# Kernel optimization log

Measured on AMD Instinct MI355X. Metric: run time of the kernel, lower is better.

## Reference

```python
import jax, jax.numpy as jnp
import numpy as np

B, C, H, W_SP = 4, 64, 64, 64
CI = C // 2  # inter_channels = 32
DEPTH = 64
EPS = 1e-5


def conv2d(x, w, b, pad=0, dil=1):
    out = jax.lax.conv_general_dilated(
        x, w, window_strides=(1, 1),
        padding=[(pad, pad), (pad, pad)],
        rhs_dilation=(dil, dil),
        dimension_numbers=('NCHW', 'OIHW', 'NCHW'))
    return out + b[None, :, None, None]


def setup_inputs() -> dict:
    key = jax.random.key(0)
    ks = iter(jax.random.split(key, 32))
    nrm = lambda shp, s=0.01: jax.random.normal(next(ks), shp, jnp.float32) * s
    inp = {
        'x': jax.random.normal(next(ks), (B, C, H, W_SP), jnp.float32),
        # NonlocalBlock params (init: normal(0, 0.01), bias 0)
        'g_w': nrm((CI, C, 1, 1)), 'g_b': jnp.zeros((CI,), jnp.float32),
        'theta_w': nrm((CI, C, 1, 1)), 'theta_b': jnp.zeros((CI,), jnp.float32),
        'phi_w': nrm((CI, C, 1, 1)), 'phi_b': jnp.zeros((CI,), jnp.float32),
        'Wz_w': nrm((C, CI, 1, 1)), 'Wz_b': jnp.zeros((C,), jnp.float32),
        'bn_g': jax.random.normal(next(ks), (C,), jnp.float32),  # normal_(W[1].weight, 0) -> std 1
        'bn_b': jnp.zeros((C,), jnp.float32),
        # ASPP params (torch default kaiming init approximated by small normals)
        'a_mean_w': nrm((DEPTH, C, 1, 1), 0.05), 'a_mean_b': jnp.zeros((DEPTH,), jnp.float32),
        'a1_w': nrm((DEPTH, C, 1, 1), 0.05), 'a1_b': jnp.zeros((DEPTH,), jnp.float32),
        'a3_w': nrm((DEPTH, C, 3, 3), 0.02), 'a3_b': jnp.zeros((DEPTH,), jnp.float32),
        'a5_w': nrm((DEPTH, C, 3, 3), 0.02), 'a5_b': jnp.zeros((DEPTH,), jnp.float32),
        'a7_w': nrm((DEPTH, C, 3, 3), 0.02), 'a7_b': jnp.zeros((DEPTH,), jnp.float32),
        'out_w': nrm((DEPTH, DEPTH * 5, 1, 1), 0.02), 'out_b': jnp.zeros((DEPTH,), jnp.float32),
    }
    return inp


def _forward(x, g_w, g_b, theta_w, theta_b, phi_w, phi_b, Wz_w, Wz_b, bn_g, bn_b,
             a_mean_w, a_mean_b, a1_w, a1_b, a3_w, a3_b, a5_w, a5_b, a7_w, a7_b,
             out_w, out_b):
    b, c, h, w = x.shape
    n = h * w
    # ---- NonlocalBlock: global self-attention ----
    g_x = conv2d(x, g_w, g_b).reshape(b, CI, n).transpose(0, 2, 1)       # [B,N,Ci]
    theta_x = conv2d(x, theta_w, theta_b).reshape(b, CI, n).transpose(0, 2, 1)  # [B,N,Ci]
    phi_x = conv2d(x, phi_w, phi_b).reshape(b, CI, n)                    # [B,Ci,N]
    f = jnp.einsum('bqc,bck->bqk', theta_x, phi_x)                       # [B,N,N]
    f_div_C = jax.nn.softmax(f, axis=2)
    y = jnp.einsum('bqk,bkc->bqc', f_div_C, g_x)                         # [B,N,Ci]
    y = y.transpose(0, 2, 1).reshape(b, CI, h, w)
    wy = conv2d(y, Wz_w, Wz_b)
    # BatchNorm (eval: running_mean=0, running_var=1)
    wy = wy * (bn_g / jnp.sqrt(1.0 + EPS))[None, :, None, None] + bn_b[None, :, None, None]
    z = wy + x
    # ---- ASPP ----
    img = jnp.mean(z, axis=(2, 3), keepdims=True)                        # [B,C,1,1]
    img = conv2d(img, a_mean_w, a_mean_b)                                # [B,D,1,1]
    img = jnp.broadcast_to(img, (b, DEPTH, h, w))  # bilinear upsample of 1x1 is constant
    b1 = conv2d(z, a1_w, a1_b)
    b3 = conv2d(z, a3_w, a3_b, pad=3, dil=3)
    b5 = conv2d(z, a5_w, a5_b, pad=5, dil=5)
    b7 = conv2d(z, a7_w, a7_b, pad=7, dil=7)
    cat = jnp.concatenate([img, b1, b3, b5, b7], axis=1)                 # [B,5D,H,W]
    return conv2d(cat, out_w, out_b)                                     # [B,D,H,W]


def reference(x, g_w, g_b, theta_w, theta_b, phi_w, phi_b, Wz_w, Wz_b, bn_g, bn_b,
              a_mean_w, a_mean_b, a1_w, a1_b, a3_w, a3_b, a5_w, a5_b, a7_w, a7_b,
              out_w, out_b):
    return _forward(x, g_w, g_b, theta_w, theta_b, phi_w, phi_b, Wz_w, Wz_b, bn_g, bn_b,
                    a_mean_w, a_mean_b, a1_w, a1_b, a3_w, a3_b, a5_w, a5_b, a7_w, a7_b,
                    out_w, out_b)
```

## Files before the change

### kernel.cpp

```cpp
#include <hip/hip_runtime.h>


typedef __attribute__((ext_vector_type(8))) short bf16x8;
typedef __attribute__((ext_vector_type(4))) short s16x4;
typedef __attribute__((ext_vector_type(4))) float f32x4;

#define MFMA(a, b, c) __builtin_amdgcn_mfma_f32_16x16x32_bf16((a), (b), (c), 0, 0, 0)

#if __has_builtin(__builtin_amdgcn_exp2f)
#define EXP2(x) __builtin_amdgcn_exp2f(x)
#else
#define EXP2(x) exp2f(x)
#endif

__device__ static inline short f2bf(float f) {
  union { float f; unsigned u; } v; v.f = f;
  unsigned r = v.u + 0x7fffu + ((v.u >> 16) & 1u);
  return (short)(r >> 16);
}
__device__ static inline s16x4 pk4(f32x4 v) {
  s16x4 r; r.x = f2bf(v.x); r.y = f2bf(v.y); r.z = f2bf(v.z); r.w = f2bf(v.w);
  return r;
}
__device__ static inline unsigned pk2(float f0, float f1) {
  union { float f; unsigned u; } a, b; a.f = f0; b.f = f1;
  return __builtin_amdgcn_perm(b.u, a.u, 0x07060302u);
}
__device__ static inline f32x4 exp24(f32x4 v) {
  f32x4 r; r.x = EXP2(v.x); r.y = EXP2(v.y); r.z = EXP2(v.z); r.w = EXP2(v.w);
  return r;
}

#define QF_PER_B 131072
#define ZPB      389376
#define LOG2E    1.4426950408889634f

__global__ __launch_bounds__(256) void k_proj(
    const float* __restrict__ x,
    const float* __restrict__ tw, const float* __restrict__ tb,
    const float* __restrict__ pw, const float* __restrict__ pb,
    const float* __restrict__ gw, const float* __restrict__ gb,
    const float* __restrict__ Wz_w, const float* __restrict__ Wz_b,
    const float* __restrict__ bn_g, const float* __restrict__ bn_b,
    unsigned short* __restrict__ thetaB, unsigned short* __restrict__ phiB,
    unsigned short* __restrict__ gB, unsigned short* __restrict__ WzF,
    float* __restrict__ bias2, float* __restrict__ zmean) {
  __shared__ float wl[2048];
  __shared__ float bl[32];
  int blk = blockIdx.x, t = threadIdx.x;
  if (blk < 192) {
    int b = blk & 3, pt = (blk >> 2) & 15, proj = blk >> 6;
    const float* w    = proj == 0 ? tw : (proj == 1 ? pw : gw);
    const float* bias = proj == 0 ? tb : (proj == 1 ? pb : gb);
    for (int i = t; i < 2048; i += 256) wl[i] = w[i];
    if (t < 32) bl[t] = bias[t];
    __syncthreads();
    int pix = pt*256 + t;
    const float* xp = x + b*64*4096 + pix;
    float acc[32];
    #pragma unroll
    for (int ci = 0; ci < 32; ++ci) acc[ci] = bl[ci];
    for (int c0 = 0; c0 < 64; c0 += 16) {
      float xv[16];
      #pragma unroll
      for (int k = 0; k < 16; ++k) xv[k] = xp[(c0 + k)*4096];
      #pragma unroll
      for (int k = 0; k < 16; ++k)
        #pragma unroll
        for (int ci = 0; ci < 32; ++ci) acc[ci] += wl[ci*64 + c0 + k] * xv[k];
    }
    if (proj == 0) {
      #pragma unroll
      for (int ci = 0; ci < 32; ++ci) acc[ci] *= LOG2E;
    }
    if (proj < 2) {
      unsigned short* base = (proj == 0 ? thetaB : phiB) + b*QF_PER_B
                             + (pix >> 4)*512 + (pix & 15)*8;
      #pragma unroll
      for (int q = 0; q < 4; ++q) {
        bf16x8 v;
        #pragma unroll
        for (int j = 0; j < 8; ++j) v[j] = f2bf(acc[q*8 + j]);
        *(bf16x8*)(base + q*128) = v;
      }
    } else {
      unsigned short* base = gB + b*QF_PER_B + (pix >> 5)*1024
                             + ((pix & 31) >> 3)*128 + (pix & 7);
      #pragma unroll
      for (int ci = 0; ci < 32; ++ci)
        base[(ci >> 4)*512 + (ci & 15)*8] = (unsigned short)f2bf(acc[ci]);
    }
  } else if (blk == 192) {
    int ct = t >> 6, lane = t & 63, quad = lane >> 4, l15 = lane & 15;
    int c = ct * 16 + l15;
    float s = bn_g[c] * rsqrtf(1.f + 1e-5f);
    bf16x8 v;
    #pragma unroll
    for (int j = 0; j < 8; ++j) v[j] = f2bf(s * Wz_w[c * 32 + quad * 8 + j]);
    *(bf16x8*)(WzF + (ct * 64 + lane) * 8) = v;
    if (t < 64) {
      float s2 = bn_g[t] * rsqrtf(1.f + 1e-5f);
      bias2[t] = s2 * Wz_b[t] + bn_b[t];
    }
  } else {
    zmean[t] = 0.f;
  }
}

__global__ __launch_bounds__(512, 4) void k_attn(
    const unsigned short* __restrict__ thetaB, const unsigned short* __restrict__ phiB,
    const unsigned short* __restrict__ gB, const unsigned short* __restrict__ WzF,
    const float* __restrict__ bias2, const float* __restrict__ x,
    unsigned short* __restrict__ z_pad, float* __restrict__ zmean,
    const float* __restrict__ out_w, const float* __restrict__ out_b,
    const float* __restrict__ a1_w, const float* __restrict__ a3_w,
    const float* __restrict__ a5_w, const float* __restrict__ a7_w,
    const float* __restrict__ a1_b, const float* __restrict__ a3_b,
    const float* __restrict__ a5_b, const float* __restrict__ a7_b,
    const float* __restrict__ am_w,
    unsigned short* __restrict__ Wfrag, float* __restrict__ am_wT,
    float* __restrict__ owT0, float* __restrict__ cbias) {
  __shared__ union {
    struct {
      float ypart[8][64][20];
      unsigned short plds[8][1152];
      unsigned short ytr[4][1280];
    } attn;
    struct { float wsm[4096]; float osm[64 * 65]; } prep;
  } sm;
  int blk = blockIdx.x, tid = threadIdx.x;
  if (blk < 512) {
    int b = blk >> 7, qblk = blk & 127;
    int kh = tid >> 6, lane = tid & 63, quad = lane >> 4, l15 = lane & 15;
    const bf16x8* thB = (const bf16x8*)(thetaB + b*QF_PER_B);
    const bf16x8* phF = (const bf16x8*)(phiB + b*QF_PER_B);
    const bf16x8* gF  = (const bf16x8*)(gB + b*QF_PER_B);
    bf16x8 th0 = thB[(qblk*2 + 0)*64 + lane];
    bf16x8 th1 = thB[(qblk*2 + 1)*64 + lane];
    bf16x8 ones;
    #pragma unroll
    for (int j = 0; j < 8; ++j) ones[j] = (short)0x3F80;
    const f32x4 z4 = {0.f, 0.f, 0.f, 0.f};
    f32x4 acc00 = z4, acc01 = z4, acc10 = z4, acc11 = z4;
    f32x4 accL0 = z4, accL1 = z4;
    unsigned short* pl = &sm.attn.plds[kh][0];
    unsigned short* r0p = pl + l15*36 + quad*4;
    unsigned short* r1p = pl + 576 + l15*36 + quad*4;
    const unsigned short* q0p = pl + l15*36 + quad*8;
    const unsigned short* q1p = pl + 576 + l15*36 + quad*8;
    int kt0 = kh*16;
    int tb0 = kt0*128 + lane;
    bf16x8 pf0 = phF[tb0], pf1 = phF[tb0 + 64];
    bf16x8 gf0 = gF[tb0],  gf1 = gF[tb0 + 64];
    for (int kt = kt0; kt < kt0 + 16; ++kt) {
      bf16x8 cp0 = pf0, cp1 = pf1, cg0 = gf0, cg1 = gf1;
      if (kt + 1 < kt0 + 16) {
        int tb = (kt + 1)*128 + lane;
        pf0 = phF[tb]; pf1 = phF[tb + 64];
        gf0 = gF[tb];  gf1 = gF[tb + 64];
      }
      f32x4 s00 = MFMA(cp0, th0, z4);
      f32x4 s10 = MFMA(cp1, th0, z4);
      f32x4 s01 = MFMA(cp0, th1, z4);
      f32x4 s11 = MFMA(cp1, th1, z4);
      f32x4 p00 = exp24(s00), p10 = exp24(s10), p01 = exp24(s01), p11 = exp24(s11);
      uint2 w0; w0.x = pk2(p00.x, p00.y); w0.y = pk2(p00.z, p00.w);
      uint2 w1; w1.x = pk2(p10.x, p10.y); w1.y = pk2(p10.z, p10.w);
      uint2 w2; w2.x = pk2(p01.x, p01.y); w2.y = pk2(p01.z, p01.w);
      uint2 w3; w3.x = pk2(p11.x, p11.y); w3.y = pk2(p11.z, p11.w);
      *(uint2*)(r0p)      = w0;
      *(uint2*)(r0p + 16) = w1;
      *(uint2*)(r1p)      = w2;
      *(uint2*)(r1p + 16) = w3;
      uint2 a0 = *(const uint2*)(q0p);
      uint2 a1 = *(const uint2*)(q0p + 4);
      uint2 b0 = *(const uint2*)(q1p);
      uint2 b1 = *(const uint2*)(q1p + 4);
      union { unsigned u[4]; bf16x8 v; } pb0c, pb1c;
      pb0c.u[0] = a0.x; pb0c.u[1] = a0.y; pb0c.u[2] = a1.x; pb0c.u[3] = a1.y;
      pb1c.u[0] = b0.x; pb1c.u[1] = b0.y; pb1c.u[2] = b1.x; pb1c.u[3] = b1.y;
      acc00 = MFMA(cg0, pb0c.v, acc00);
      acc01 = MFMA(cg1, pb0c.v, acc01);
      acc10 = MFMA(cg0, pb1c.v, acc10);
      acc11 = MFMA(cg1, pb1c.v, acc11);
      accL0 = MFMA(ones, pb0c.v, accL0);
      accL1 = MFMA(ones, pb1c.v, accL1);
    }
    float* yp = &sm.attn.ypart[kh][lane][0];
    *(f32x4*)(yp + 0)  = acc00;
    *(f32x4*)(yp + 4)  = acc01;
    *(f32x4*)(yp + 8)  = acc10;
    *(f32x4*)(yp + 12) = acc11;
    yp[16] = accL0.x; yp[17] = accL1.x;
    __syncthreads();
    if (kh >= 4) return;
    int ct = kh;
    f32x4 a00 = z4, a01 = z4, a10 = z4, a11 = z4;
    float l0 = 0.f, l1 = 0.f;
    #pragma unroll
    for (int k = 0; k < 8; ++k) {
      const float* q = &sm.attn.ypart[k][lane][0];
      a00 += *(const f32x4*)(q + 0);
      a01 += *(const f32x4*)(q + 4);
      a10 += *(const f32x4*)(q + 8);
      a11 += *(const f32x4*)(q + 12);
      l0 += q[16]; l1 += q[17];
    }
    float r0 = 1.f / l0, r1 = 1.f / l1;
    a00 *= r0; a01 *= r0; a10 *= r1; a11 *= r1;
    unsigned short* yl = &sm.attn.ytr[ct][0];
    *(s16x4*)(yl + l15*40 + quad*4)             = pk4(a00);
    *(s16x4*)(yl + l15*40 + 16 + quad*4)        = pk4(a01);
    *(s16x4*)(yl + (16 + l15)*40 + quad*4)      = pk4(a10);
    *(s16x4*)(yl + (16 + l15)*40 + 16 + quad*4) = pk4(a11);
    bf16x8 y0 = *(const bf16x8*)(yl + l15*40 + quad*8);
    bf16x8 y1 = *(const bf16x8*)(yl + (16 + l15)*40 + quad*8);
    bf16x8 wf = ((const bf16x8*)WzF)[ct*64 + lane];
    f32x4 zq0 = MFMA(wf, y0, z4);
    f32x4 zq1 = MFMA(wf, y1, z4);
    int c0 = ct*16 + quad*4;
    f32x4 b2 = *(const f32x4*)(bias2 + c0);
    int q0i = qblk * 32;
    const float* xp0 = x + (b*64 + c0)*4096 + q0i + l15;
    f32x4 s0, s1;
    s0.x = zq0.x + b2.x + xp0[0];
    s0.y = zq0.y + b2.y + xp0[4096];
    s0.z = zq0.z + b2.z + xp0[8192];
    s0.w = zq0.w + b2.w + xp0[12288];
    s1.x = zq1.x + b2.x + xp0[16];
    s1.y = zq1.y + b2.y + xp0[4096 + 16];
    s1.z = zq1.z + b2.z + xp0[8192 + 16];
    s1.w = zq1.w + b2.w + xp0[12288 + 16];
    {
      int q = q0i + l15, h = q >> 6, w = q & 63;
      *(s16x4*)(z_pad + b*ZPB + ((h + 7)*78 + (w + 7))*64 + c0) = pk4(s0);
      q = q0i + 16 + l15; h = q >> 6; w = q & 63;
      *(s16x4*)(z_pad + b*ZPB + ((h + 7)*78 + (w + 7))*64 + c0) = pk4(s1);
    }
    f32x4 zs = s0 + s1;
    #pragma unroll
    for (int m = 1; m < 16; m <<= 1) {
      zs.x += __shfl_xor(zs.x, m);
      zs.y += __shfl_xor(zs.y, m);
      zs.z += __shfl_xor(zs.z, m);
      zs.w += __shfl_xor(zs.w, m);
    }
    if (l15 == 0) {
      atomicAdd(zmean + b*64 + c0 + 0, zs.x);
      atomicAdd(zmean + b*64 + c0 + 1, zs.y);
      atomicAdd(zmean + b*64 + c0 + 2, zs.z);
      atomicAdd(zmean + b*64 + c0 + 3, zs.w);
    }
  } else if (blk < 1012) {
    int hb = blk - 512;
    int b = hb / 125, loc = hb - b * 125;
    int i = loc * 512 + tid;
    if (i >= 63616) return;
    int px = i >> 5, dw = i & 31;
    int row, col;
    if (px < 1092) {
      int r = px / 78; col = px - r * 78;
      row = (r < 7) ? r : r + 64;
    } else {
      int j = px - 1092;
      int r = j / 14; int c = j - r * 14;
      row = r + 7; col = (c < 7) ? c : c + 64;
    }
    ((unsigned*)z_pad)[b * (ZPB / 2) + (row * 78 + col) * 32 + dw] = 0u;
  } else if (blk < 1040) {
    int tap = blk - 1012;
    const float* w; int goff, kyx = 0, ksq = 9;
    if (tap == 0)      { w = a1_w; goff = 64;  ksq = 1; }
    else if (tap < 10) { w = a3_w; goff = 128; kyx = tap - 1; }
    else if (tap < 19) { w = a5_w; goff = 192; kyx = tap - 10; }
    else               { w = a7_w; goff = 256; kyx = tap - 19; }
    for (int i = tid; i < 4096; i += 512) {
      sm.prep.wsm[i] = w[i * ksq + kyx];
      int d = i >> 6, m = i & 63;
      sm.prep.osm[d * 65 + m] = out_w[d * 320 + goff + m];
    }
    __syncthreads();
    int dt = (tid >> 6) & 3, lane = tid & 63, quad = lane >> 4, l15 = lane & 15;
    int d = dt * 16 + l15;
    float acc[16];
    #pragma unroll
    for (int k = 0; k < 16; ++k) acc[k] = 0.f;
    const float* orow = sm.prep.osm + d * 65;
    int c0 = quad * 8;
    for (int m = 0; m < 64; ++m) {
      float o = orow[m];
      const float* wr = sm.prep.wsm + m * 64 + c0;
      #pragma unroll
      for (int cc = 0; cc < 2; ++cc)
        #pragma unroll
        for (int j = 0; j < 8; ++j)
          acc[cc * 8 + j] += o * wr[cc * 32 + j];
    }
    #pragma unroll
    for (int cc = 0; cc < 2; ++cc) {
      bf16x8 v;
      #pragma unroll
      for (int j = 0; j < 8; ++j) v[j] = f2bf(acc[cc * 8 + j]);
      *(bf16x8*)(Wfrag + (((tap * 4 + dt) * 2 + cc) * 64 + lane) * 8) = v;
    }
  } else {
    for (int i = tid; i < 4096; i += 512) {
      int d = i >> 6, c = i & 63;
      am_wT[c * 64 + d] = am_w[i];
      owT0[c * 64 + d] = out_w[d * 320 + c];
    }
    if (tid < 64) {
      float r = out_b[tid];
      const float* ow = out_w + tid * 320;
      for (int m = 0; m < 64; ++m)
        r += ow[64 + m] * a1_b[m] + ow[128 + m] * a3_b[m]
           + ow[192 + m] * a5_b[m] + ow[256 + m] * a7_b[m];
      cbias[tid] = r;
    }
  }
}

__global__ __launch_bounds__(256, 4) void k_conv(
    const unsigned short* __restrict__ z_pad, const unsigned short* __restrict__ Wfrag,
    const float* __restrict__ zmean, const float* __restrict__ am_wT,
    const float* __restrict__ am_b, const float* __restrict__ owT0,
    const float* __restrict__ cbias, float* __restrict__ out) {
  static constexpr int DYt[28] = {0, -3,-3,-3,0,0,0,3,3,3,
                                     -5,-5,-5,0,0,0,5,5,5,
                                     -7,-7,-7,0,0,0,7,7,7};
  static constexpr int DXt[28] = {0, -3,0,3,-3,0,3,-3,0,3,
                                     -5,0,5,-5,0,5,-5,0,5,
                                     -7,0,7,-7,0,7,-7,0,7};
  int blk = blockIdx.x;
  int b = blk >> 6, h = blk & 63;
  int tid = threadIdx.x;
  int wave = tid >> 6, lane = tid & 63, quad = lane >> 4, l15 = lane & 15;
  int dt2 = wave >> 1, wt2 = wave & 1;
  float zml = zmean[b*64 + lane] * (1.f / 4096.f);
  float img = am_b[lane];
  for (int c = 0; c < 64; ++c) img += am_wT[c*64 + lane] * __shfl(zml, c);
  float cbd = cbias[lane];
  for (int dd = 0; dd < 64; ++dd) cbd += owT0[dd*64 + lane] * __shfl(img, dd);
  const unsigned short* zb = z_pad + b*ZPB + ((h + 7)*78 + 7)*64 + quad*8;
  const bf16x8* wfp = (const bf16x8*)Wfrag + lane;
  int d0 = dt2*2 + 0, d1 = dt2*2 + 1;
  const f32x4 z4 = {0.f, 0.f, 0.f, 0.f};
  f32x4 acc00 = z4, acc01 = z4, acc10 = z4, acc11 = z4;
  int col0 = ((wt2*2 + 0)*16 + l15)*64;
  int col1 = ((wt2*2 + 1)*16 + l15)*64;
  bf16x8 zf0 = *(const bf16x8*)(zb + (DYt[0]*78 + DXt[0])*64 + col0);
  bf16x8 zf1 = *(const bf16x8*)(zb + (DYt[0]*78 + DXt[0])*64 + col1);
  #pragma unroll
  for (int idx = 0; idx < 56; ++idx) {
    int tap = idx >> 1, cc = idx & 1;
    bf16x8 c0v = zf0, c1v = zf1;
    if (idx < 55) {
      int ntap = (idx + 1) >> 1, ncc = (idx + 1) & 1;
      const unsigned short* nz = zb + (DYt[ntap]*78 + DXt[ntap])*64 + ncc*32;
      zf0 = *(const bf16x8*)(nz + col0);
      zf1 = *(const bf16x8*)(nz + col1);
    }
    bf16x8 wf0 = wfp[((tap*4 + d0)*2 + cc)*64];
    bf16x8 wf1 = wfp[((tap*4 + d1)*2 + cc)*64];
    acc00 = MFMA(wf0, c0v, acc00);
    acc01 = MFMA(wf0, c1v, acc01);
    acc10 = MFMA(wf1, c0v, acc10);
    acc11 = MFMA(wf1, c1v, acc11);
  }
  int dd0 = d0*16 + quad*4, dd1 = d1*16 + quad*4;
  f32x4 cb0v, cb1v;
  cb0v.x = __shfl(cbd, dd0 + 0); cb0v.y = __shfl(cbd, dd0 + 1);
  cb0v.z = __shfl(cbd, dd0 + 2); cb0v.w = __shfl(cbd, dd0 + 3);
  cb1v.x = __shfl(cbd, dd1 + 0); cb1v.y = __shfl(cbd, dd1 + 1);
  cb1v.z = __shfl(cbd, dd1 + 2); cb1v.w = __shfl(cbd, dd1 + 3);
  acc00 += cb0v; acc01 += cb0v; acc10 += cb1v; acc11 += cb1v;
  float* ob = out + b*262144 + h*64;
  int w0 = (wt2*2 + 0)*16 + l15, w1 = (wt2*2 + 1)*16 + l15;
  ob[(dd0 + 0)*4096 + w0] = acc00.x;
  ob[(dd0 + 1)*4096 + w0] = acc00.y;
  ob[(dd0 + 2)*4096 + w0] = acc00.z;
  ob[(dd0 + 3)*4096 + w0] = acc00.w;
  ob[(dd0 + 0)*4096 + w1] = acc01.x;
  ob[(dd0 + 1)*4096 + w1] = acc01.y;
  ob[(dd0 + 2)*4096 + w1] = acc01.z;
  ob[(dd0 + 3)*4096 + w1] = acc01.w;
  ob[(dd1 + 0)*4096 + w0] = acc10.x;
  ob[(dd1 + 1)*4096 + w0] = acc10.y;
  ob[(dd1 + 2)*4096 + w0] = acc10.z;
  ob[(dd1 + 3)*4096 + w0] = acc10.w;
  ob[(dd1 + 0)*4096 + w1] = acc11.x;
  ob[(dd1 + 1)*4096 + w1] = acc11.y;
  ob[(dd1 + 2)*4096 + w1] = acc11.z;
  ob[(dd1 + 3)*4096 + w1] = acc11.w;
}

extern "C" void kernel_launch(void* const* d_in, const int* in_sizes, int n_in,
                              void* d_out, int out_size, void* d_ws, size_t ws_size,
                              hipStream_t stream) {
  const float* x    = (const float*)d_in[0];
  const float* g_w  = (const float*)d_in[1];
  const float* g_b  = (const float*)d_in[2];
  const float* th_w = (const float*)d_in[3];
  const float* th_b = (const float*)d_in[4];
  const float* ph_w = (const float*)d_in[5];
  const float* ph_b = (const float*)d_in[6];
  const float* Wz_w = (const float*)d_in[7];
  const float* Wz_b = (const float*)d_in[8];
  const float* bn_g = (const float*)d_in[9];
  const float* bn_b = (const float*)d_in[10];
  const float* am_w = (const float*)d_in[11];
  const float* am_b = (const float*)d_in[12];
  const float* a1_w = (const float*)d_in[13];
  const float* a1_b = (const float*)d_in[14];
  const float* a3_w = (const float*)d_in[15];
  const float* a3_b = (const float*)d_in[16];
  const float* a5_w = (const float*)d_in[17];
  const float* a5_b = (const float*)d_in[18];
  const float* a7_w = (const float*)d_in[19];
  const float* a7_b = (const float*)d_in[20];
  const float* out_w = (const float*)d_in[21];
  const float* out_b = (const float*)d_in[22];
  float* out = (float*)d_out;
  char* ws = (char*)d_ws;
  unsigned short* thetaB = (unsigned short*)(ws + 0);
  unsigned short* phiB   = (unsigned short*)(ws + 1048576);
  unsigned short* gB     = (unsigned short*)(ws + 2097152);
  unsigned short* z_pad  = (unsigned short*)(ws + 3145728);
  unsigned short* Wfrag  = (unsigned short*)(ws + 6260736);
  unsigned short* WzF    = (unsigned short*)(ws + 6490112);
  float* zmean           = (float*)(ws + 6494208);
  float* bias2           = (float*)(ws + 6495232);
  float* am_wT           = (float*)(ws + 6495488);
  float* owT0            = (float*)(ws + 6511872);
  float* cbias           = (float*)(ws + 6528256);

  k_proj<<<dim3(194), dim3(256), 0, stream>>>(
      x, th_w, th_b, ph_w, ph_b, g_w, g_b, Wz_w, Wz_b, bn_g, bn_b,
      thetaB, phiB, gB, WzF, bias2, zmean);
  k_attn<<<dim3(1041), dim3(512), 0, stream>>>(
      thetaB, phiB, gB, WzF, bias2, x, z_pad, zmean,
      out_w, out_b, a1_w, a3_w, a5_w, a7_w, a1_b, a3_b, a5_b, a7_b, am_w,
      Wfrag, am_wT, owT0, cbias);
  k_conv<<<dim3(256), dim3(256), 0, stream>>>(z_pad, Wfrag, zmean, am_wT, am_b,
                                              owT0, cbias, out);
}
```

Before: 189.5 us.

## Move weight prep and padding to proj kernel, pack attn partials, deepen conv prefetch

```diff
diff --git a/kernel.cpp b/kernel.cpp
--- a/kernel.cpp
+++ b/kernel.cpp
@@ -25,6 +25,18 @@
 __device__ static inline unsigned pk2(float f0, float f1) {
   union { float f; unsigned u; } a, b; a.f = f0; b.f = f1;
   return __builtin_amdgcn_perm(b.u, a.u, 0x07060302u);
+}
+__device__ static inline float unlo(unsigned d) {
+  union { unsigned u; float f; } v; v.u = d << 16; return v.f;
+}
+__device__ static inline float unhi(unsigned d) {
+  union { unsigned u; float f; } v; v.u = d & 0xffff0000u; return v.f;
+}
+__device__ static inline unsigned fasu(float f) {
+  union { float f; unsigned u; } v; v.f = f; return v.u;
+}
+__device__ static inline float uasf(unsigned u) {
+  union { unsigned u; float f; } v; v.u = u; return v.f;
 }
 __device__ static inline f32x4 exp24(f32x4 v) {
   f32x4 r; r.x = EXP2(v.x); r.y = EXP2(v.y); r.z = EXP2(v.z); r.w = EXP2(v.w);
@@ -42,24 +54,35 @@
     const float* __restrict__ gw, const float* __restrict__ gb,
     const float* __restrict__ Wz_w, const float* __restrict__ Wz_b,
     const float* __restrict__ bn_g, const float* __restrict__ bn_b,
+    const float* __restrict__ out_w, const float* __restrict__ out_b,
+    const float* __restrict__ a1_w, const float* __restrict__ a3_w,
+    const float* __restrict__ a5_w, const float* __restrict__ a7_w,
+    const float* __restrict__ a1_b, const float* __restrict__ a3_b,
+    const float* __restrict__ a5_b, const float* __restrict__ a7_b,
+    const float* __restrict__ am_w,
     unsigned short* __restrict__ thetaB, unsigned short* __restrict__ phiB,
     unsigned short* __restrict__ gB, unsigned short* __restrict__ WzF,
-    float* __restrict__ bias2, float* __restrict__ zmean) {
-  __shared__ float wl[2048];
-  __shared__ float bl[32];
+    float* __restrict__ bias2, float* __restrict__ zmean,
+    unsigned* __restrict__ zp, unsigned short* __restrict__ Wfrag,
+    float* __restrict__ am_wT, float* __restrict__ owT0,
+    float* __restrict__ cbias) {
+  __shared__ union {
+    struct { float wl[2048]; float bl[32]; } qkv;
+    struct { float wsm[4096]; float osm[64 * 65]; } prep;
+  } sm;
   int blk = blockIdx.x, t = threadIdx.x;
   if (blk < 192) {
     int b = blk & 3, pt = (blk >> 2) & 15, proj = blk >> 6;
     const float* w    = proj == 0 ? tw : (proj == 1 ? pw : gw);
     const float* bias = proj == 0 ? tb : (proj == 1 ? pb : gb);
-    for (int i = t; i < 2048; i += 256) wl[i] = w[i];
-    if (t < 32) bl[t] = bias[t];
+    for (int i = t; i < 2048; i += 256) sm.qkv.wl[i] = w[i];
+    if (t < 32) sm.qkv.bl[t] = bias[t];
     __syncthreads();
     int pix = pt*256 + t;
     const float* xp = x + b*64*4096 + pix;
     float acc[32];
     #pragma unroll
-    for (int ci = 0; ci < 32; ++ci) acc[ci] = bl[ci];
+    for (int ci = 0; ci < 32; ++ci) acc[ci] = sm.qkv.bl[ci];
     for (int c0 = 0; c0 < 64; c0 += 16) {
       float xv[16];
       #pragma unroll
@@ -67,7 +90,7 @@
       #pragma unroll
       for (int k = 0; k < 16; ++k)
         #pragma unroll
-        for (int ci = 0; ci < 32; ++ci) acc[ci] += wl[ci*64 + c0 + k] * xv[k];
+        for (int ci = 0; ci < 32; ++ci) acc[ci] += sm.qkv.wl[ci*64 + c0 + k] * xv[k];
     }
     if (proj == 0) {
       #pragma unroll
@@ -98,163 +121,15 @@
     #pragma unroll
     for (int j = 0; j < 8; ++j) v[j] = f2bf(s * Wz_w[c * 32 + quad * 8 + j]);
     *(bf16x8*)(WzF + (ct * 64 + lane) * 8) = v;
+    zmean[t] = 0.f;
     if (t < 64) {
       float s2 = bn_g[t] * rsqrtf(1.f + 1e-5f);
       bias2[t] = s2 * Wz_b[t] + bn_b[t];
     }
-  } else {
-    zmean[t] = 0.f;
-  }
-}
-
-__global__ __launch_bounds__(512, 4) void k_attn(
-    const unsigned short* __restrict__ thetaB, const unsigned short* __restrict__ phiB,
-    const unsigned short* __restrict__ gB, const unsigned short* __restrict__ WzF,
-    const float* __restrict__ bias2, const float* __restrict__ x,
-    unsigned short* __restrict__ z_pad, float* __restrict__ zmean,
-    const float* __restrict__ out_w, const float* __restrict__ out_b,
-    const float* __restrict__ a1_w, const float* __restrict__ a3_w,
-    const float* __restrict__ a5_w, const float* __restrict__ a7_w,
-    const float* __restrict__ a1_b, const float* __restrict__ a3_b,
-    const float* __restrict__ a5_b, const float* __restrict__ a7_b,
-    const float* __restrict__ am_w,
-    unsigned short* __restrict__ Wfrag, float* __restrict__ am_wT,
-    float* __restrict__ owT0, float* __restrict__ cbias) {
-  __shared__ union {
-    struct {
-      float ypart[8][64][20];
-      unsigned short plds[8][1152];
-      unsigned short ytr[4][1280];
-    } attn;
-    struct { float wsm[4096]; float osm[64 * 65]; } prep;
-  } sm;
-  int blk = blockIdx.x, tid = threadIdx.x;
-  if (blk < 512) {
-    int b = blk >> 7, qblk = blk & 127;
-    int kh = tid >> 6, lane = tid & 63, quad = lane >> 4, l15 = lane & 15;
-    const bf16x8* thB = (const bf16x8*)(thetaB + b*QF_PER_B);
-    const bf16x8* phF = (const bf16x8*)(phiB + b*QF_PER_B);
-    const bf16x8* gF  = (const bf16x8*)(gB + b*QF_PER_B);
-    bf16x8 th0 = thB[(qblk*2 + 0)*64 + lane];
-    bf16x8 th1 = thB[(qblk*2 + 1)*64 + lane];
-    bf16x8 ones;
-    #pragma unroll
-    for (int j = 0; j < 8; ++j) ones[j] = (short)0x3F80;
-    const f32x4 z4 = {0.f, 0.f, 0.f, 0.f};
-    f32x4 acc00 = z4, acc01 = z4, acc10 = z4, acc11 = z4;
-    f32x4 accL0 = z4, accL1 = z4;
-    unsigned short* pl = &sm.attn.plds[kh][0];
-    unsigned short* r0p = pl + l15*36 + quad*4;
-    unsigned short* r1p = pl + 576 + l15*36 + quad*4;
-    const unsigned short* q0p = pl + l15*36 + quad*8;
-    const unsigned short* q1p = pl + 576 + l15*36 + quad*8;
-    int kt0 = kh*16;
-    int tb0 = kt0*128 + lane;
-    bf16x8 pf0 = phF[tb0], pf1 = phF[tb0 + 64];
-    bf16x8 gf0 = gF[tb0],  gf1 = gF[tb0 + 64];
-    for (int kt = kt0; kt < kt0 + 16; ++kt) {
-      bf16x8 cp0 = pf0, cp1 = pf1, cg0 = gf0, cg1 = gf1;
-      if (kt + 1 < kt0 + 16) {
-        int tb = (kt + 1)*128 + lane;
-        pf0 = phF[tb]; pf1 = phF[tb + 64];
-        gf0 = gF[tb];  gf1 = gF[tb + 64];
-      }
-      f32x4 s00 = MFMA(cp0, th0, z4);
-      f32x4 s10 = MFMA(cp1, th0, z4);
-      f32x4 s01 = MFMA(cp0, th1, z4);
-      f32x4 s11 = MFMA(cp1, th1, z4);
-      f32x4 p00 = exp24(s00), p10 = exp24(s10), p01 = exp24(s01), p11 = exp24(s11);
-      uint2 w0; w0.x = pk2(p00.x, p00.y); w0.y = pk2(p00.z, p00.w);
-      uint2 w1; w1.x = pk2(p10.x, p10.y); w1.y = pk2(p10.z, p10.w);
-      uint2 w2; w2.x = pk2(p01.x, p01.y); w2.y = pk2(p01.z, p01.w);
-      uint2 w3; w3.x = pk2(p11.x, p11.y); w3.y = pk2(p11.z, p11.w);
-      *(uint2*)(r0p)      = w0;
-      *(uint2*)(r0p + 16) = w1;
-      *(uint2*)(r1p)      = w2;
-      *(uint2*)(r1p + 16) = w3;
-      uint2 a0 = *(const uint2*)(q0p);
-      uint2 a1 = *(const uint2*)(q0p + 4);
-      uint2 b0 = *(const uint2*)(q1p);
-      uint2 b1 = *(const uint2*)(q1p + 4);
-      union { unsigned u[4]; bf16x8 v; } pb0c, pb1c;
-      pb0c.u[0] = a0.x; pb0c.u[1] = a0.y; pb0c.u[2] = a1.x; pb0c.u[3] = a1.y;
-      pb1c.u[0] = b0.x; pb1c.u[1] = b0.y; pb1c.u[2] = b1.x; pb1c.u[3] = b1.y;
-      acc00 = MFMA(cg0, pb0c.v, acc00);
-      acc01 = MFMA(cg1, pb0c.v, acc01);
-      acc10 = MFMA(cg0, pb1c.v, acc10);
-      acc11 = MFMA(cg1, pb1c.v, acc11);
-      accL0 = MFMA(ones, pb0c.v, accL0);
-      accL1 = MFMA(ones, pb1c.v, accL1);
-    }
-    float* yp = &sm.attn.ypart[kh][lane][0];
-    *(f32x4*)(yp + 0)  = acc00;
-    *(f32x4*)(yp + 4)  = acc01;
-    *(f32x4*)(yp + 8)  = acc10;
-    *(f32x4*)(yp + 12) = acc11;
-    yp[16] = accL0.x; yp[17] = accL1.x;
-    __syncthreads();
-    if (kh >= 4) return;
-    int ct = kh;
-    f32x4 a00 = z4, a01 = z4, a10 = z4, a11 = z4;
-    float l0 = 0.f, l1 = 0.f;
-    #pragma unroll
-    for (int k = 0; k < 8; ++k) {
-      const float* q = &sm.attn.ypart[k][lane][0];
-      a00 += *(const f32x4*)(q + 0);
-      a01 += *(const f32x4*)(q + 4);
-      a10 += *(const f32x4*)(q + 8);
-      a11 += *(const f32x4*)(q + 12);
-      l0 += q[16]; l1 += q[17];
-    }
-    float r0 = 1.f / l0, r1 = 1.f / l1;
-    a00 *= r0; a01 *= r0; a10 *= r1; a11 *= r1;
-    unsigned short* yl = &sm.attn.ytr[ct][0];
-    *(s16x4*)(yl + l15*40 + quad*4)             = pk4(a00);
-    *(s16x4*)(yl + l15*40 + 16 + quad*4)        = pk4(a01);
-    *(s16x4*)(yl + (16 + l15)*40 + quad*4)      = pk4(a10);
-    *(s16x4*)(yl + (16 + l15)*40 + 16 + quad*4) = pk4(a11);
-    bf16x8 y0 = *(const bf16x8*)(yl + l15*40 + quad*8);
-    bf16x8 y1 = *(const bf16x8*)(yl + (16 + l15)*40 + quad*8);
-    bf16x8 wf = ((const bf16x8*)WzF)[ct*64 + lane];
-    f32x4 zq0 = MFMA(wf, y0, z4);
-    f32x4 zq1 = MFMA(wf, y1, z4);
-    int c0 = ct*16 + quad*4;
-    f32x4 b2 = *(const f32x4*)(bias2 + c0);
-    int q0i = qblk * 32;
-    const float* xp0 = x + (b*64 + c0)*4096 + q0i + l15;
-    f32x4 s0, s1;
-    s0.x = zq0.x + b2.x + xp0[0];
-    s0.y = zq0.y + b2.y + xp0[4096];
-    s0.z = zq0.z + b2.z + xp0[8192];
-    s0.w = zq0.w + b2.w + xp0[12288];
-    s1.x = zq1.x + b2.x + xp0[16];
-    s1.y = zq1.y + b2.y + xp0[4096 + 16];
-    s1.z = zq1.z + b2.z + xp0[8192 + 16];
-    s1.w = zq1.w + b2.w + xp0[12288 + 16];
-    {
-      int q = q0i + l15, h = q >> 6, w = q & 63;
-      *(s16x4*)(z_pad + b*ZPB + ((h + 7)*78 + (w + 7))*64 + c0) = pk4(s0);
-      q = q0i + 16 + l15; h = q >> 6; w = q & 63;
-      *(s16x4*)(z_pad + b*ZPB + ((h + 7)*78 + (w + 7))*64 + c0) = pk4(s1);
-    }
-    f32x4 zs = s0 + s1;
-    #pragma unroll
-    for (int m = 1; m < 16; m <<= 1) {
-      zs.x += __shfl_xor(zs.x, m);
-      zs.y += __shfl_xor(zs.y, m);
-      zs.z += __shfl_xor(zs.z, m);
-      zs.w += __shfl_xor(zs.w, m);
-    }
-    if (l15 == 0) {
-      atomicAdd(zmean + b*64 + c0 + 0, zs.x);
-      atomicAdd(zmean + b*64 + c0 + 1, zs.y);
-      atomicAdd(zmean + b*64 + c0 + 2, zs.z);
-      atomicAdd(zmean + b*64 + c0 + 3, zs.w);
-    }
-  } else if (blk < 1012) {
-    int hb = blk - 512;
-    int b = hb / 125, loc = hb - b * 125;
-    int i = loc * 512 + tid;
+  } else if (blk < 1189) {
+    int hb = blk - 193;
+    int b = hb / 249, loc = hb - b * 249;
+    int i = loc * 256 + t;
     if (i >= 63616) return;
     int px = i >> 5, dw = i & 31;
     int row, col;
@@ -266,21 +141,21 @@
       int r = j / 14; int c = j - r * 14;
       row = r + 7; col = (c < 7) ? c : c + 64;
     }
-    ((unsigned*)z_pad)[b * (ZPB / 2) + (row * 78 + col) * 32 + dw] = 0u;
-  } else if (blk < 1040) {
-    int tap = blk - 1012;
+    zp[b * (ZPB / 2) + (row * 78 + col) * 32 + dw] = 0u;
+  } else if (blk < 1217) {
+    int tap = blk - 1189;
     const float* w; int goff, kyx = 0, ksq = 9;
     if (tap == 0)      { w = a1_w; goff = 64;  ksq = 1; }
     else if (tap < 10) { w = a3_w; goff = 128; kyx = tap - 1; }
     else if (tap < 19) { w = a5_w; goff = 192; kyx = tap - 10; }
     else               { w = a7_w; goff = 256; kyx = tap - 19; }
-    for (int i = tid; i < 4096; i += 512) {
+    for (int i = t; i < 4096; i += 256) {
       sm.prep.wsm[i] = w[i * ksq + kyx];
       int d = i >> 6, m = i & 63;
       sm.prep.osm[d * 65 + m] = out_w[d * 320 + goff + m];
     }
     __syncthreads();
-    int dt = (tid >> 6) & 3, lane = tid & 63, quad = lane >> 4, l15 = lane & 15;
+    int dt = t >> 6, lane = t & 63, quad = lane >> 4, l15 = lane & 15;
     int d = dt * 16 + l15;
     float acc[16];
     #pragma unroll
@@ -304,19 +179,162 @@
       *(bf16x8*)(Wfrag + (((tap * 4 + dt) * 2 + cc) * 64 + lane) * 8) = v;
     }
   } else {
-    for (int i = tid; i < 4096; i += 512) {
+    for (int i = t; i < 4096; i += 256) {
       int d = i >> 6, c = i & 63;
       am_wT[c * 64 + d] = am_w[i];
       owT0[c * 64 + d] = out_w[d * 320 + c];
     }
-    if (tid < 64) {
-      float r = out_b[tid];
-      const float* ow = out_w + tid * 320;
+    if (t < 64) {
+      float r = out_b[t];
+      const float* ow = out_w + t * 320;
       for (int m = 0; m < 64; ++m)
         r += ow[64 + m] * a1_b[m] + ow[128 + m] * a3_b[m]
            + ow[192 + m] * a5_b[m] + ow[256 + m] * a7_b[m];
-      cbias[tid] = r;
-    }
+      cbias[t] = r;
+    }
+  }
+}
+
+__global__ __launch_bounds__(512, 4) void k_attn(
+    const unsigned short* __restrict__ thetaB, const unsigned short* __restrict__ phiB,
+    const unsigned short* __restrict__ gB, const unsigned short* __restrict__ WzF,
+    const float* __restrict__ bias2, const float* __restrict__ x,
+    unsigned short* __restrict__ z_pad, float* __restrict__ zmean) {
+  __shared__ struct {
+    unsigned ypk[8][10][64];
+    __align__(16) unsigned short plds[8][1152];
+  } sm;
+  int blk = blockIdx.x;
+  int b = blk >> 7, qblk = blk & 127;
+  int tid = threadIdx.x;
+  int kh = tid >> 6, lane = tid & 63, quad = lane >> 4, l15 = lane & 15;
+  const bf16x8* thB = (const bf16x8*)(thetaB + b*QF_PER_B);
+  const bf16x8* phF = (const bf16x8*)(phiB + b*QF_PER_B);
+  const bf16x8* gF  = (const bf16x8*)(gB + b*QF_PER_B);
+  bf16x8 th0 = thB[(qblk*2 + 0)*64 + lane];
+  bf16x8 th1 = thB[(qblk*2 + 1)*64 + lane];
+  bf16x8 ones;
+  #pragma unroll
+  for (int j = 0; j < 8; ++j) ones[j] = (short)0x3F80;
+  const f32x4 z4 = {0.f, 0.f, 0.f, 0.f};
+  f32x4 acc00 = z4, acc01 = z4, acc10 = z4, acc11 = z4;
+  f32x4 accL0 = z4, accL1 = z4;
+  unsigned short* pl = &sm.plds[kh][0];
+  unsigned short* r0p = pl + l15*36 + quad*4;
+  unsigned short* r1p = pl + 576 + l15*36 + quad*4;
+  const unsigned short* q0p = pl + l15*36 + quad*8;
+  const unsigned short* q1p = pl + 576 + l15*36 + quad*8;
+  int kt0 = kh*16;
+  int tb0 = kt0*128 + lane;
+  bf16x8 pf0 = phF[tb0], pf1 = phF[tb0 + 64];
+  bf16x8 gf0 = gF[tb0],  gf1 = gF[tb0 + 64];
+  for (int kt = kt0; kt < kt0 + 16; ++kt) {
+    bf16x8 cp0 = pf0, cp1 = pf1, cg0 = gf0, cg1 = gf1;
+    if (kt + 1 < kt0 + 16) {
+      int tb = (kt + 1)*128 + lane;
+      pf0 = phF[tb]; pf1 = phF[tb + 64];
+      gf0 = gF[tb];  gf1 = gF[tb + 64];
+    }
+    f32x4 s00 = MFMA(cp0, th0, z4);
+    f32x4 s10 = MFMA(cp1, th0, z4);
+    f32x4 s01 = MFMA(cp0, th1, z4);
+    f32x4 s11 = MFMA(cp1, th1, z4);
+    f32x4 p00 = exp24(s00), p10 = exp24(s10), p01 = exp24(s01), p11 = exp24(s11);
+    uint2 w0; w0.x = pk2(p00.x, p00.y); w0.y = pk2(p00.z, p00.w);
+    uint2 w1; w1.x = pk2(p10.x, p10.y); w1.y = pk2(p10.z, p10.w);
+    uint2 w2; w2.x = pk2(p01.x, p01.y); w2.y = pk2(p01.z, p01.w);
+    uint2 w3; w3.x = pk2(p11.x, p11.y); w3.y = pk2(p11.z, p11.w);
+    *(uint2*)(r0p)      = w0;
+    *(uint2*)(r0p + 16) = w1;
+    *(uint2*)(r1p)      = w2;
+    *(uint2*)(r1p + 16) = w3;
+    uint2 a0 = *(const uint2*)(q0p);
+    uint2 a1 = *(const uint2*)(q0p + 4);
+    uint2 b0 = *(const uint2*)(q1p);
+    uint2 b1 = *(const uint2*)(q1p + 4);
+    union { unsigned u[4]; bf16x8 v; } pb0c, pb1c;
+    pb0c.u[0] = a0.x; pb0c.u[1] = a0.y; pb0c.u[2] = a1.x; pb0c.u[3] = a1.y;
+    pb1c.u[0] = b0.x; pb1c.u[1] = b0.y; pb1c.u[2] = b1.x; pb1c.u[3] = b1.y;
+    acc00 = MFMA(cg0, pb0c.v, acc00);
+    acc01 = MFMA(cg1, pb0c.v, acc01);
+    acc10 = MFMA(cg0, pb1c.v, acc10);
+    acc11 = MFMA(cg1, pb1c.v, acc11);
+    accL0 = MFMA(ones, pb0c.v, accL0);
+    accL1 = MFMA(ones, pb1c.v, accL1);
+  }
+  {
+    unsigned* yp = &sm.ypk[kh][0][lane];
+    yp[0*64] = pk2(acc00.x, acc00.y);
+    yp[1*64] = pk2(acc00.z, acc00.w);
+    yp[2*64] = pk2(acc01.x, acc01.y);
+    yp[3*64] = pk2(acc01.z, acc01.w);
+    yp[4*64] = pk2(acc10.x, acc10.y);
+    yp[5*64] = pk2(acc10.z, acc10.w);
+    yp[6*64] = pk2(acc11.x, acc11.y);
+    yp[7*64] = pk2(acc11.z, acc11.w);
+    yp[8*64] = fasu(accL0.x);
+    yp[9*64] = fasu(accL1.x);
+  }
+  __syncthreads();
+  if (kh >= 4) return;
+  int ct = kh;
+  f32x4 a00 = z4, a01 = z4, a10 = z4, a11 = z4;
+  float l0 = 0.f, l1 = 0.f;
+  #pragma unroll
+  for (int k = 0; k < 8; ++k) {
+    const unsigned* q = &sm.ypk[k][0][lane];
+    unsigned d0v = q[0], d1v = q[64], d2v = q[128], d3v = q[192];
+    unsigned d4v = q[256], d5v = q[320], d6v = q[384], d7v = q[448];
+    a00.x += unlo(d0v); a00.y += unhi(d0v); a00.z += unlo(d1v); a00.w += unhi(d1v);
+    a01.x += unlo(d2v); a01.y += unhi(d2v); a01.z += unlo(d3v); a01.w += unhi(d3v);
+    a10.x += unlo(d4v); a10.y += unhi(d4v); a10.z += unlo(d5v); a10.w += unhi(d5v);
+    a11.x += unlo(d6v); a11.y += unhi(d6v); a11.z += unlo(d7v); a11.w += unhi(d7v);
+    l0 += uasf(q[512]); l1 += uasf(q[576]);
+  }
+  float r0 = 1.f / l0, r1 = 1.f / l1;
+  a00 *= r0; a01 *= r0; a10 *= r1; a11 *= r1;
+  unsigned short* yl = &sm.plds[0][0] + ct*1280;
+  *(s16x4*)(yl + l15*40 + quad*4)             = pk4(a00);
+  *(s16x4*)(yl + l15*40 + 16 + quad*4)        = pk4(a01);
+  *(s16x4*)(yl + (16 + l15)*40 + quad*4)      = pk4(a10);
+  *(s16x4*)(yl + (16 + l15)*40 + 16 + quad*4) = pk4(a11);
+  bf16x8 y0 = *(const bf16x8*)(yl + l15*40 + quad*8);
+  bf16x8 y1 = *(const bf16x8*)(yl + (16 + l15)*40 + quad*8);
+  bf16x8 wf = ((const bf16x8*)WzF)[ct*64 + lane];
+  f32x4 zq0 = MFMA(wf, y0, z4);
+  f32x4 zq1 = MFMA(wf, y1, z4);
+  int c0 = ct*16 + quad*4;
+  f32x4 b2 = *(const f32x4*)(bias2 + c0);
+  int q0i = qblk * 32;
+  const float* xp0 = x + (b*64 + c0)*4096 + q0i + l15;
+  f32x4 s0, s1;
+  s0.x = zq0.x + b2.x + xp0[0];
+  s0.y = zq0.y + b2.y + xp0[4096];
+  s0.z = zq0.z + b2.z + xp0[8192];
+  s0.w = zq0.w + b2.w + xp0[12288];
+  s1.x = zq1.x + b2.x + xp0[16];
+  s1.y = zq1.y + b2.y + xp0[4096 + 16];
+  s1.z = zq1.z + b2.z + xp0[8192 + 16];
+  s1.w = zq1.w + b2.w + xp0[12288 + 16];
+  {
+    int q = q0i + l15, h = q >> 6, w = q & 63;
+    *(s16x4*)(z_pad + b*ZPB + ((h + 7)*78 + (w + 7))*64 + c0) = pk4(s0);
+    q = q0i + 16 + l15; h = q >> 6; w = q & 63;
+    *(s16x4*)(z_pad + b*ZPB + ((h + 7)*78 + (w + 7))*64 + c0) = pk4(s1);
+  }
+  f32x4 zs = s0 + s1;
+  #pragma unroll
+  for (int m = 1; m < 16; m <<= 1) {
+    zs.x += __shfl_xor(zs.x, m);
+    zs.y += __shfl_xor(zs.y, m);
+    zs.z += __shfl_xor(zs.z, m);
+    zs.w += __shfl_xor(zs.w, m);
+  }
+  if (l15 == 0) {
+    atomicAdd(zmean + b*64 + c0 + 0, zs.x);
+    atomicAdd(zmean + b*64 + c0 + 1, zs.y);
+    atomicAdd(zmean + b*64 + c0 + 2, zs.z);
+    atomicAdd(zmean + b*64 + c0 + 3, zs.w);
   }
 }
 
@@ -348,24 +366,32 @@
   f32x4 acc00 = z4, acc01 = z4, acc10 = z4, acc11 = z4;
   int col0 = ((wt2*2 + 0)*16 + l15)*64;
   int col1 = ((wt2*2 + 1)*16 + l15)*64;
-  bf16x8 zf0 = *(const bf16x8*)(zb + (DYt[0]*78 + DXt[0])*64 + col0);
-  bf16x8 zf1 = *(const bf16x8*)(zb + (DYt[0]*78 + DXt[0])*64 + col1);
+  bf16x8 zq0[4], zq1[4], wq0[4], wq1[4];
+  #pragma unroll
+  for (int p = 0; p < 4; ++p) {
+    int tap = p >> 1, cc = p & 1;
+    const unsigned short* nz = zb + (DYt[tap]*78 + DXt[tap])*64 + cc*32;
+    zq0[p] = *(const bf16x8*)(nz + col0);
+    zq1[p] = *(const bf16x8*)(nz + col1);
+    wq0[p] = wfp[((tap*4 + d0)*2 + cc)*64];
+    wq1[p] = wfp[((tap*4 + d1)*2 + cc)*64];
+  }
   #pragma unroll
   for (int idx = 0; idx < 56; ++idx) {
-    int tap = idx >> 1, cc = idx & 1;
-    bf16x8 c0v = zf0, c1v = zf1;
-    if (idx < 55) {
-      int ntap = (idx + 1) >> 1, ncc = (idx + 1) & 1;
+    int slot = idx & 3;
+    bf16x8 zc0 = zq0[slot], zc1 = zq1[slot], wc0 = wq0[slot], wc1 = wq1[slot];
+    if (idx + 4 < 56) {
+      int ntap = (idx + 4) >> 1, ncc = (idx + 4) & 1;
       const unsigned short* nz = zb + (DYt[ntap]*78 + DXt[ntap])*64 + ncc*32;
-      zf0 = *(const bf16x8*)(nz + col0);
-      zf1 = *(const bf16x8*)(nz + col1);
-    }
-    bf16x8 wf0 = wfp[((tap*4 + d0)*2 + cc)*64];
-    bf16x8 wf1 = wfp[((tap*4 + d1)*2 + cc)*64];
-    acc00 = MFMA(wf0, c0v, acc00);
-    acc01 = MFMA(wf0, c1v, acc01);
-    acc10 = MFMA(wf1, c0v, acc10);
-    acc11 = MFMA(wf1, c1v, acc11);
+      zq0[slot] = *(const bf16x8*)(nz + col0);
+      zq1[slot] = *(const bf16x8*)(nz + col1);
+      wq0[slot] = wfp[((ntap*4 + d0)*2 + ncc)*64];
+      wq1[slot] = wfp[((ntap*4 + d1)*2 + ncc)*64];
+    }
+    acc00 = MFMA(wc0, zc0, acc00);
+    acc01 = MFMA(wc0, zc1, acc01);
+    acc10 = MFMA(wc1, zc0, acc10);
+    acc11 = MFMA(wc1, zc1, acc11);
   }
   int dd0 = d0*16 + quad*4, dd1 = d1*16 + quad*4;
   f32x4 cb0v, cb1v;
@@ -434,13 +460,13 @@
   float* owT0            = (float*)(ws + 6511872);
   float* cbias           = (float*)(ws + 6528256);
 
-  k_proj<<<dim3(194), dim3(256), 0, stream>>>(
+  k_proj<<<dim3(1218), dim3(256), 0, stream>>>(
       x, th_w, th_b, ph_w, ph_b, g_w, g_b, Wz_w, Wz_b, bn_g, bn_b,
-      thetaB, phiB, gB, WzF, bias2, zmean);
-  k_attn<<<dim3(1041), dim3(512), 0, stream>>>(
-      thetaB, phiB, gB, WzF, bias2, x, z_pad, zmean,
       out_w, out_b, a1_w, a3_w, a5_w, a7_w, a1_b, a3_b, a5_b, a7_b, am_w,
-      Wfrag, am_wT, owT0, cbias);
+      thetaB, phiB, gB, WzF, bias2, zmean,
+      (unsigned*)z_pad, Wfrag, am_wT, owT0, cbias);
+  k_attn<<<dim3(512), dim3(512), 0, stream>>>(thetaB, phiB, gB, WzF, bias2, x,
+                                              z_pad, zmean);
   k_conv<<<dim3(256), dim3(256), 0, stream>>>(z_pad, Wfrag, zmean, am_wT, am_b,
                                               owT0, cbias, out);
 }
```

New measurement: 180.7 us. 4.6% less time.
